# Optimization experiments

Hardware: AMD Instinct MI355X
Metric: run time of the kernel (lower is better)

The kernel has to match this reference:

```python
import jax, jax.numpy as jnp
import numpy as np

B, N, C, H = 8, 1024, 768, 12
HD = C // H
SCALE = HD ** -0.5
LAMBD = 4.0
N_ITERS = 5


def setup_inputs() -> dict:
    key = jax.random.key(0)
    k1, k2, k3, k4, k5 = jax.random.split(key, 5)
    x = jax.random.normal(k1, (B, N, C), dtype=jnp.float32)
    W_qkv = jax.random.normal(k2, (C, 2 * C), dtype=jnp.float32) * (C ** -0.5)
    b_qkv = jax.random.normal(k3, (2 * C,), dtype=jnp.float32) * 0.02
    W_proj = jax.random.normal(k4, (C, C), dtype=jnp.float32) * (C ** -0.5)
    b_proj = jax.random.normal(k5, (C,), dtype=jnp.float32) * 0.02
    return {"x": x, "W_qkv": W_qkv, "b_qkv": b_qkv, "W_proj": W_proj, "b_proj": b_proj}


def _soft_threshold(s, t):
    # (s - t) where s >= t, (s + t) where s <= -t, else 0  (matches the int-mask math)
    return jnp.where(s >= t, s - t, jnp.where(s <= -t, s + t, jnp.zeros_like(s)))


def reference(x, W_qkv, b_qkv, W_proj, b_proj):
    qkv = (x @ W_qkv + b_qkv).reshape(B, N, 2, H, HD)
    qkv = jnp.transpose(qkv, (2, 0, 3, 1, 4))  # [2, B, H, N, HD]
    k, v = qkv[0], qkv[1]

    # mu: [B, H, 1, 1], scalar per (batch, head): N*C/4 / ||k||_1
    mu = (N * C / 4.0) / jnp.sum(jnp.abs(k), axis=(-1, -2), keepdims=True)
    lm = LAMBD * mu

    l = jnp.zeros((B, H, N, HD), dtype=x.dtype)
    y = jnp.zeros((B, H, N, HD), dtype=x.dtype)

    for _ in range(N_ITERS):
        s = _soft_threshold(k - l + y / mu, lm)
        k2 = k - s - y / mu
        attn = jax.nn.softmax(jnp.einsum('bhnd,bhmd->bhnm', k2, k2) * SCALE, axis=-1)
        l = jnp.einsum('bhnm,bhmd->bhnd', attn, v)
        y = y + mu * (k - l - s)

    s = _soft_threshold(k - l + y / mu, lm)
    k2 = k - s - y / mu
    attn = jax.nn.softmax(jnp.einsum('bhnd,bhmd->bhnm', k2, k2) * SCALE, axis=-1)
    out = jnp.einsum('bhnm,bhmd->bhnd', attn, v)  # [B, H, N, HD]

    out = jnp.transpose(out, (0, 2, 1, 3)).reshape(B, N, C)
    out = out @ W_proj + b_proj
    return out, attn
```

## Files before the change

### kernel.cpp

```cpp
#include <hip/hip_runtime.h>

#define B_   8
#define N_   1024
#define C_   768
#define H_   12
#define HD_  64
#define BH_  96
#define SCALE_ 0.125f
#define NIT_ 5

typedef __attribute__((ext_vector_type(8))) short bfrag;
typedef __attribute__((ext_vector_type(4))) float facc;

__device__ __forceinline__ unsigned short bfhi(float x)
{
    return (unsigned short)(__float_as_uint(x) >> 16);
}
__device__ __forceinline__ unsigned short bflo(float x)
{
    const unsigned hu = __float_as_uint(x) & 0xffff0000u;
    return (unsigned short)(__float_as_uint(x - __uint_as_float(hu)) >> 16);
}
__device__ __forceinline__ bfrag pack_hi(float4 a, float4 b)
{
    bfrag r;
    r[0] = (short)bfhi(a.x); r[1] = (short)bfhi(a.y);
    r[2] = (short)bfhi(a.z); r[3] = (short)bfhi(a.w);
    r[4] = (short)bfhi(b.x); r[5] = (short)bfhi(b.y);
    r[6] = (short)bfhi(b.z); r[7] = (short)bfhi(b.w);
    return r;
}
__device__ __forceinline__ bfrag pack_lo(float4 a, float4 b)
{
    bfrag r;
    r[0] = (short)bflo(a.x); r[1] = (short)bflo(a.y);
    r[2] = (short)bflo(a.z); r[3] = (short)bflo(a.w);
    r[4] = (short)bflo(b.x); r[5] = (short)bflo(b.y);
    r[6] = (short)bflo(b.z); r[7] = (short)bflo(b.w);
    return r;
}

__global__ __launch_bounds__(256)
void split_flat(const float* __restrict__ In,
                unsigned short* __restrict__ Oh, unsigned short* __restrict__ Ol)
{
    const size_t i = ((size_t)blockIdx.x * 256 + threadIdx.x) * 8;
    const float4 a = *(const float4*)(In + i);
    const float4 b = *(const float4*)(In + i + 4);
    *(bfrag*)(Oh + i) = pack_hi(a, b);
    *(bfrag*)(Ol + i) = pack_lo(a, b);
}

__global__ __launch_bounds__(256)
void split_wt(const float* __restrict__ W, int ncols,
// ... 291 lines not shown

__global__ __launch_bounds__(256)
void musum(const float* __restrict__ Kb, float* __restrict__ mu)
{
    const int bh = blockIdx.x;
    const int tid = threadIdx.x;
    const float* p = Kb + (size_t)bh * (N_ * HD_);
    float s = 0.0f;
    for (int i = tid; i < N_ * HD_; i += 256) s += fabsf(p[i]);
    for (int off = 32; off; off >>= 1) s += __shfl_down(s, off, 64);
    __shared__ float red[4];
    if ((tid & 63) == 0) red[tid >> 6] = s;
    __syncthreads();
    if (tid == 0)
        mu[bh] = (float)(N_ * C_ / 4.0) / (red[0] + red[1] + red[2] + red[3]);
}

__global__ __launch_bounds__(256)
void ew_fused(const float* __restrict__ Kb, const float* __restrict__ Lb,
              float* __restrict__ Yb, const float* __restrict__ mu,
              float* __restrict__ K2b,
              unsigned short* __restrict__ K2h, unsigned short* __restrict__ K2l,
              int upd)
{
    const int i = blockIdx.x * 256 + threadIdx.x;
    const int bh = i >> 16;
    const float m = mu[bh];
    const float lm = 4.0f * m;
    const float kv = Kb[i];
    float k2;
    if (upd) {
        const float lv = Lb[i];
        const float y = 2.0f * Yb[i] + m * (K2b[i] - lv);
        Yb[i] = y;
        const float yom = y / m;
        const float t = kv - lv + yom;
        const float s = (t >= lm) ? (t - lm) : ((t <= -lm) ? (t + lm) : 0.0f);
        k2 = kv - s - yom;
    } else {
        Yb[i] = 0.0f;
        const float t = kv;
        const float s = (t >= lm) ? (t - lm) : ((t <= -lm) ? (t + lm) : 0.0f);
        k2 = kv - s;
    }
    K2b[i] = k2;
    K2h[i] = bfhi(k2);
    K2l[i] = bflo(k2);
}

__global__ __launch_bounds__(256)
void vt_split(const float* __restrict__ Vb,
              unsigned short* __restrict__ Vth, unsigned short* __restrict__ Vtl)
{
    __shared__ float Ts[64][68];
    const int tid = threadIdx.x;
    const int bh = blockIdx.y;
    const int n0 = blockIdx.x * 64;
    const float* vb = Vb + ((size_t)bh * N_ + n0) * HD_;

    {
        int e = tid;
#pragma unroll
        for (int t = 0; t < 4; ++t, e += 256) {
            const int r = e >> 4, c4 = (e & 15) << 2;
            *(float4*)&Ts[r][c4] = *(const float4*)(vb + r * HD_ + c4);
        }
    }
    __syncthreads();

#pragma unroll
    for (int t = 0; t < 2; ++t) {
        const int idx = t * 2048 + tid * 8;
        const int d = idx >> 6, c = idx & 63;
        bfrag h8, l8;
#pragma unroll
        for (int q = 0; q < 8; ++q) {
            const float v = Ts[c + q][d];
            h8[q] = (short)bfhi(v);
            l8[q] = (short)bflo(v);
        }
        const size_t go = ((size_t)bh * HD_ + d) * N_ + n0 + c;
        *(bfrag*)(Vth + go) = h8;
        *(bfrag*)(Vtl + go) = l8;
    }
}

__global__ __launch_bounds__(256)
void flash(const unsigned short* __restrict__ K2h, const unsigned short* __restrict__ K2l,
           const unsigned short* __restrict__ Vth, const unsigned short* __restrict__ Vtl,
           float* __restrict__ Lout, float* __restrict__ Mrow, float* __restrict__ Zrow,
           unsigned short* __restrict__ Lbh, unsigned short* __restrict__ Lbl, int wsplit)
{
    __shared__ short Kh[64][72];
    __shared__ short Kl[64][72];
    __shared__ short Vh[64][72];
    __shared__ short Vl[64][72];
    short (&Ph)[64][72] = Kh;
    short (&Pl)[64][72] = Kl;

    const int tid  = threadIdx.x;
    const int lane = tid & 63;
    const int w    = tid >> 6;
    const int g    = lane >> 4;
    const int r16  = lane & 15;
    const int bh   = blockIdx.y;
    const int q0   = blockIdx.x * 128;

    const unsigned short* kh = K2h + (size_t)bh * (N_ * HD_);
    const unsigned short* kl = K2l + (size_t)bh * (N_ * HD_);
    const unsigned short* vh = Vth + (size_t)bh * (N_ * HD_);
    const unsigned short* vl = Vtl + (size_t)bh * (N_ * HD_);

    const size_t qoffA = (size_t)(q0 + 16 * w + r16) * HD_ + 8 * g;
    const size_t qoffB = (size_t)(q0 + 64 + 16 * w + r16) * HD_ + 8 * g;
    const bfrag qhA0 = *(const bfrag*)(kh + qoffA);
    const bfrag qhA1 = *(const bfrag*)(kh + qoffA + 32);
    const bfrag qlA0 = *(const bfrag*)(kl + qoffA);
    const bfrag qlA1 = *(const bfrag*)(kl + qoffA + 32);
    const bfrag qhB0 = *(const bfrag*)(kh + qoffB);
    const bfrag qhB1 = *(const bfrag*)(kh + qoffB + 32);
    const bfrag qlB0 = *(const bfrag*)(kl + qoffB);
    const bfrag qlB1 = *(const bfrag*)(kl + qoffB + 32);

    const int i0 = tid * 8,        r0 = i0 >> 6, cc0 = i0 & 63;
    const int i1 = 2048 + tid * 8, r1 = i1 >> 6, cc1 = i1 & 63;

    bfrag pk0 = *(const bfrag*)(kh + i0);
    bfrag pk1 = *(const bfrag*)(kh + i1);
    bfrag pm0 = *(const bfrag*)(kl + i0);
    bfrag pm1 = *(const bfrag*)(kl + i1);

    float mrA0 = -1e30f, mrA1 = -1e30f, mrA2 = -1e30f, mrA3 = -1e30f;
    float zrA0 = 0.0f,  zrA1 = 0.0f,  zrA2 = 0.0f,  zrA3 = 0.0f;
    float mrB0 = -1e30f, mrB1 = -1e30f, mrB2 = -1e30f, mrB3 = -1e30f;
    float zrB0 = 0.0f,  zrB1 = 0.0f,  zrB2 = 0.0f,  zrB3 = 0.0f;
    facc oA0 = {0.f, 0.f, 0.f, 0.f};
    facc oA1 = {0.f, 0.f, 0.f, 0.f};
    facc oA2 = {0.f, 0.f, 0.f, 0.f};
    facc oA3 = {0.f, 0.f, 0.f, 0.f};
    facc oB0 = {0.f, 0.f, 0.f, 0.f};
    facc oB1 = {0.f, 0.f, 0.f, 0.f};
    facc oB2 = {0.f, 0.f, 0.f, 0.f};
    facc oB3 = {0.f, 0.f, 0.f, 0.f};

    for (int kt = 0; kt < 16; ++kt) {
        __syncthreads();
        *(bfrag*)&Kh[r0][cc0] = pk0;  *(bfrag*)&Kh[r1][cc1] = pk1;
        *(bfrag*)&Kl[r0][cc0] = pm0;  *(bfrag*)&Kl[r1][cc1] = pm1;
        const bfrag tv0 = *(const bfrag*)(vh + (size_t)r0 * N_ + kt * 64 + cc0);
        const bfrag tv1 = *(const bfrag*)(vh + (size_t)r1 * N_ + kt * 64 + cc1);
        const bfrag tw0 = *(const bfrag*)(vl + (size_t)r0 * N_ + kt * 64 + cc0);
        const bfrag tw1 = *(const bfrag*)(vl + (size_t)r1 * N_ + kt * 64 + cc1);
        if (kt + 1 < 16) {
            const size_t gn = (size_t)(kt + 1) * 4096;
            pk0 = *(const bfrag*)(kh + gn + i0);
            pk1 = *(const bfrag*)(kh + gn + i1);
            pm0 = *(const bfrag*)(kl + gn + i0);
            pm1 = *(const bfrag*)(kl + gn + i1);
        }
        __syncthreads();

        facc sA0 = {0.f, 0.f, 0.f, 0.f};
        facc sA1 = {0.f, 0.f, 0.f, 0.f};
        facc sA2 = {0.f, 0.f, 0.f, 0.f};
        facc sA3 = {0.f, 0.f, 0.f, 0.f};
        facc sB0 = {0.f, 0.f, 0.f, 0.f};
        facc sB1 = {0.f, 0.f, 0.f, 0.f};
        facc sB2 = {0.f, 0.f, 0.f, 0.f};
        facc sB3 = {0.f, 0.f, 0.f, 0.f};
        {
            bfrag b0 = *(const bfrag*)&Kh[r16][8 * g];
            bfrag b1 = *(const bfrag*)&Kh[r16][32 + 8 * g];
            bfrag c0 = *(const bfrag*)&Kl[r16][8 * g];
            bfrag c1 = *(const bfrag*)&Kl[r16][32 + 8 * g];
            sA0 = __builtin_amdgcn_mfma_f32_16x16x32_bf16(qhA0, b0, sA0, 0, 0, 0);
            sA0 = __builtin_amdgcn_mfma_f32_16x16x32_bf16(qlA0, b0, sA0, 0, 0, 0);
            sA0 = __builtin_amdgcn_mfma_f32_16x16x32_bf16(qhA0, c0, sA0, 0, 0, 0);
            sA0 = __builtin_amdgcn_mfma_f32_16x16x32_bf16(qhA1, b1, sA0, 0, 0, 0);
            sA0 = __builtin_amdgcn_mfma_f32_16x16x32_bf16(qlA1, b1, sA0, 0, 0, 0);
            sA0 = __builtin_amdgcn_mfma_f32_16x16x32_bf16(qhA1, c1, sA0, 0, 0, 0);
            sB0 = __builtin_amdgcn_mfma_f32_16x16x32_bf16(qhB0, b0, sB0, 0, 0, 0);
            sB0 = __builtin_amdgcn_mfma_f32_16x16x32_bf16(qlB0, b0, sB0, 0, 0, 0);
            sB0 = __builtin_amdgcn_mfma_f32_16x16x32_bf16(qhB0, c0, sB0, 0, 0, 0);
            sB0 = __builtin_amdgcn_mfma_f32_16x16x32_bf16(qhB1, b1, sB0, 0, 0, 0);
            sB0 = __builtin_amdgcn_mfma_f32_16x16x32_bf16(qlB1, b1, sB0, 0, 0, 0);
// ... 111 lines not shown
        }
        const float mnB0 = fmaxf(mrB0, mt0), mnB1 = fmaxf(mrB1, mt1);
        const float mnB2 = fmaxf(mrB2, mt2), mnB3 = fmaxf(mrB3, mt3);
        const float aB0 = __expf(mrB0 - mnB0), aB1 = __expf(mrB1 - mnB1);
        const float aB2 = __expf(mrB2 - mnB2), aB3 = __expf(mrB3 - mnB3);
        mrB0 = mnB0; mrB1 = mnB1; mrB2 = mnB2; mrB3 = mnB3;

        const float paB0 = __expf(sB0.x - mnB0), paB1 = __expf(sB0.y - mnB1);
        const float paB2 = __expf(sB0.z - mnB2), paB3 = __expf(sB0.w - mnB3);
        const float pbB0 = __expf(sB1.x - mnB0), pbB1 = __expf(sB1.y - mnB1);
        const float pbB2 = __expf(sB1.z - mnB2), pbB3 = __expf(sB1.w - mnB3);
        const float pcB0 = __expf(sB2.x - mnB0), pcB1 = __expf(sB2.y - mnB1);
        const float pcB2 = __expf(sB2.z - mnB2), pcB3 = __expf(sB2.w - mnB3);
        const float pdB0 = __expf(sB3.x - mnB0), pdB1 = __expf(sB3.y - mnB1);
        const float pdB2 = __expf(sB3.z - mnB2), pdB3 = __expf(sB3.w - mnB3);

        float zsB0 = paB0 + pbB0 + pcB0 + pdB0;
        float zsB1 = paB1 + pbB1 + pcB1 + pdB1;
        float zsB2 = paB2 + pbB2 + pcB2 + pdB2;
        float zsB3 = paB3 + pbB3 + pcB3 + pdB3;
        for (int off = 8; off; off >>= 1) {
            zsB0 += __shfl_xor(zsB0, off, 16);
            zsB1 += __shfl_xor(zsB1, off, 16);
            zsB2 += __shfl_xor(zsB2, off, 16);
            zsB3 += __shfl_xor(zsB3, off, 16);
        }
        zrB0 = zrB0 * aB0 + zsB0;  zrB1 = zrB1 * aB1 + zsB1;
        zrB2 = zrB2 * aB2 + zsB2;  zrB3 = zrB3 * aB3 + zsB3;
        oB0.x *= aB0; oB0.y *= aB1; oB0.z *= aB2; oB0.w *= aB3;
        oB1.x *= aB0; oB1.y *= aB1; oB1.z *= aB2; oB1.w *= aB3;
        oB2.x *= aB0; oB2.y *= aB1; oB2.z *= aB2; oB2.w *= aB3;
        oB3.x *= aB0; oB3.y *= aB1; oB3.z *= aB2; oB3.w *= aB3;

        *(bfrag*)&Vh[r0][cc0] = tv0;  *(bfrag*)&Vh[r1][cc1] = tv1;
        *(bfrag*)&Vl[r0][cc0] = tw0;  *(bfrag*)&Vl[r1][cc1] = tw1;

        __syncthreads();

        const int pr = 16 * w + 4 * g;
        Ph[pr + 0][r16]      = (short)bfhi(paA0); Pl[pr + 0][r16]      = (short)bflo(paA0);
        Ph[pr + 1][r16]      = (short)bfhi(paA1); Pl[pr + 1][r16]      = (short)bflo(paA1);
        Ph[pr + 2][r16]      = (short)bfhi(paA2); Pl[pr + 2][r16]      = (short)bflo(paA2);
        Ph[pr + 3][r16]      = (short)bfhi(paA3); Pl[pr + 3][r16]      = (short)bflo(paA3);
        Ph[pr + 0][16 + r16] = (short)bfhi(pbA0); Pl[pr + 0][16 + r16] = (short)bflo(pbA0);
        Ph[pr + 1][16 + r16] = (short)bfhi(pbA1); Pl[pr + 1][16 + r16] = (short)bflo(pbA1);
        Ph[pr + 2][16 + r16] = (short)bfhi(pbA2); Pl[pr + 2][16 + r16] = (short)bflo(pbA2);
        Ph[pr + 3][16 + r16] = (short)bfhi(pbA3); Pl[pr + 3][16 + r16] = (short)bflo(pbA3);
        Ph[pr + 0][32 + r16] = (short)bfhi(pcA0); Pl[pr + 0][32 + r16] = (short)bflo(pcA0);
        Ph[pr + 1][32 + r16] = (short)bfhi(pcA1); Pl[pr + 1][32 + r16] = (short)bflo(pcA1);
        Ph[pr + 2][32 + r16] = (short)bfhi(pcA2); Pl[pr + 2][32 + r16] = (short)bflo(pcA2);
        Ph[pr + 3][32 + r16] = (short)bfhi(pcA3); Pl[pr + 3][32 + r16] = (short)bflo(pcA3);
        Ph[pr + 0][48 + r16] = (short)bfhi(pdA0); Pl[pr + 0][48 + r16] = (short)bflo(pdA0);
        Ph[pr + 1][48 + r16] = (short)bfhi(pdA1); Pl[pr + 1][48 + r16] = (short)bflo(pdA1);
        Ph[pr + 2][48 + r16] = (short)bfhi(pdA2); Pl[pr + 2][48 + r16] = (short)bflo(pdA2);
        Ph[pr + 3][48 + r16] = (short)bfhi(pdA3); Pl[pr + 3][48 + r16] = (short)bflo(pdA3);
        __builtin_amdgcn_wave_barrier();
        {
            const bfrag ph0 = *(const bfrag*)&Ph[16 * w + r16][8 * g];
            const bfrag ph1 = *(const bfrag*)&Ph[16 * w + r16][32 + 8 * g];
            const bfrag pl0 = *(const bfrag*)&Pl[16 * w + r16][8 * g];
            const bfrag pl1 = *(const bfrag*)&Pl[16 * w + r16][32 + 8 * g];
            {
                bfrag b0 = *(const bfrag*)&Vh[r16][8 * g];
                bfrag b1 = *(const bfrag*)&Vh[r16][32 + 8 * g];
                bfrag c0 = *(const bfrag*)&Vl[r16][8 * g];
                bfrag c1 = *(const bfrag*)&Vl[r16][32 + 8 * g];
                oA0 = __builtin_amdgcn_mfma_f32_16x16x32_bf16(ph0, b0, oA0, 0, 0, 0);
                oA0 = __builtin_amdgcn_mfma_f32_16x16x32_bf16(pl0, b0, oA0, 0, 0, 0);
                oA0 = __builtin_amdgcn_mfma_f32_16x16x32_bf16(ph0, c0, oA0, 0, 0, 0);
                oA0 = __builtin_amdgcn_mfma_f32_16x16x32_bf16(ph1, b1, oA0, 0, 0, 0);
                oA0 = __builtin_amdgcn_mfma_f32_16x16x32_bf16(pl1, b1, oA0, 0, 0, 0);
                oA0 = __builtin_amdgcn_mfma_f32_16x16x32_bf16(ph1, c1, oA0, 0, 0, 0);
            }
            {
                bfrag b0 = *(const bfrag*)&Vh[16 + r16][8 * g];
                bfrag b1 = *(const bfrag*)&Vh[16 + r16][32 + 8 * g];
                bfrag c0 = *(const bfrag*)&Vl[16 + r16][8 * g];
                bfrag c1 = *(const bfrag*)&Vl[16 + r16][32 + 8 * g];
                oA1 = __builtin_amdgcn_mfma_f32_16x16x32_bf16(ph0, b0, oA1, 0, 0, 0);
                oA1 = __builtin_amdgcn_mfma_f32_16x16x32_bf16(pl0, b0, oA1, 0, 0, 0);
                oA1 = __builtin_amdgcn_mfma_f32_16x16x32_bf16(ph0, c0, oA1, 0, 0, 0);
                oA1 = __builtin_amdgcn_mfma_f32_16x16x32_bf16(ph1, b1, oA1, 0, 0, 0);
                oA1 = __builtin_amdgcn_mfma_f32_16x16x32_bf16(pl1, b1, oA1, 0, 0, 0);
                oA1 = __builtin_amdgcn_mfma_f32_16x16x32_bf16(ph1, c1, oA1, 0, 0, 0);
            }
            {
                bfrag b0 = *(const bfrag*)&Vh[32 + r16][8 * g];
                bfrag b1 = *(const bfrag*)&Vh[32 + r16][32 + 8 * g];
                bfrag c0 = *(const bfrag*)&Vl[32 + r16][8 * g];
                bfrag c1 = *(const bfrag*)&Vl[32 + r16][32 + 8 * g];
                oA2 = __builtin_amdgcn_mfma_f32_16x16x32_bf16(ph0, b0, oA2, 0, 0, 0);
                oA2 = __builtin_amdgcn_mfma_f32_16x16x32_bf16(pl0, b0, oA2, 0, 0, 0);
                oA2 = __builtin_amdgcn_mfma_f32_16x16x32_bf16(ph0, c0, oA2, 0, 0, 0);
                oA2 = __builtin_amdgcn_mfma_f32_16x16x32_bf16(ph1, b1, oA2, 0, 0, 0);
                oA2 = __builtin_amdgcn_mfma_f32_16x16x32_bf16(pl1, b1, oA2, 0, 0, 0);
                oA2 = __builtin_amdgcn_mfma_f32_16x16x32_bf16(ph1, c1, oA2, 0, 0, 0);
            }
            {
                bfrag b0 = *(const bfrag*)&Vh[48 + r16][8 * g];
                bfrag b1 = *(const bfrag*)&Vh[48 + r16][32 + 8 * g];
                bfrag c0 = *(const bfrag*)&Vl[48 + r16][8 * g];
                bfrag c1 = *(const bfrag*)&Vl[48 + r16][32 + 8 * g];
                oA3 = __builtin_amdgcn_mfma_f32_16x16x32_bf16(ph0, b0, oA3, 0, 0, 0);
                oA3 = __builtin_amdgcn_mfma_f32_16x16x32_bf16(pl0, b0, oA3, 0, 0, 0);
                oA3 = __builtin_amdgcn_mfma_f32_16x16x32_bf16(ph0, c0, oA3, 0, 0, 0);
                oA3 = __builtin_amdgcn_mfma_f32_16x16x32_bf16(ph1, b1, oA3, 0, 0, 0);
                oA3 = __builtin_amdgcn_mfma_f32_16x16x32_bf16(pl1, b1, oA3, 0, 0, 0);
                oA3 = __builtin_amdgcn_mfma_f32_16x16x32_bf16(ph1, c1, oA3, 0, 0, 0);
            }
        }
        __builtin_amdgcn_wave_barrier();

        Ph[pr + 0][r16]      = (short)bfhi(paB0); Pl[pr + 0][r16]      = (short)bflo(paB0);
        Ph[pr + 1][r16]      = (short)bfhi(paB1); Pl[pr + 1][r16]      = (short)bflo(paB1);
        Ph[pr + 2][r16]      = (short)bfhi(paB2); Pl[pr + 2][r16]      = (short)bflo(paB2);
        Ph[pr + 3][r16]      = (short)bfhi(paB3); Pl[pr + 3][r16]      = (short)bflo(paB3);
        Ph[pr + 0][16 + r16] = (short)bfhi(pbB0); Pl[pr + 0][16 + r16] = (short)bflo(pbB0);
        Ph[pr + 1][16 + r16] = (short)bfhi(pbB1); Pl[pr + 1][16 + r16] = (short)bflo(pbB1);
        Ph[pr + 2][16 + r16] = (short)bfhi(pbB2); Pl[pr + 2][16 + r16] = (short)bflo(pbB2);
        Ph[pr + 3][16 + r16] = (short)bfhi(pbB3); Pl[pr + 3][16 + r16] = (short)bflo(pbB3);
        Ph[pr + 0][32 + r16] = (short)bfhi(pcB0); Pl[pr + 0][32 + r16] = (short)bflo(pcB0);
        Ph[pr + 1][32 + r16] = (short)bfhi(pcB1); Pl[pr + 1][32 + r16] = (short)bflo(pcB1);
        Ph[pr + 2][32 + r16] = (short)bfhi(pcB2); Pl[pr + 2][32 + r16] = (short)bflo(pcB2);
        Ph[pr + 3][32 + r16] = (short)bfhi(pcB3); Pl[pr + 3][32 + r16] = (short)bflo(pcB3);
        Ph[pr + 0][48 + r16] = (short)bfhi(pdB0); Pl[pr + 0][48 + r16] = (short)bflo(pdB0);
        Ph[pr + 1][48 + r16] = (short)bfhi(pdB1); Pl[pr + 1][48 + r16] = (short)bflo(pdB1);
        Ph[pr + 2][48 + r16] = (short)bfhi(pdB2); Pl[pr + 2][48 + r16] = (short)bflo(pdB2);
        Ph[pr + 3][48 + r16] = (short)bfhi(pdB3); Pl[pr + 3][48 + r16] = (short)bflo(pdB3);
        __builtin_amdgcn_wave_barrier();
        {
            const bfrag ph0 = *(const bfrag*)&Ph[16 * w + r16][8 * g];
            const bfrag ph1 = *(const bfrag*)&Ph[16 * w + r16][32 + 8 * g];
            const bfrag pl0 = *(const bfrag*)&Pl[16 * w + r16][8 * g];
            const bfrag pl1 = *(const bfrag*)&Pl[16 * w + r16][32 + 8 * g];
            {
                bfrag b0 = *(const bfrag*)&Vh[r16][8 * g];
                bfrag b1 = *(const bfrag*)&Vh[r16][32 + 8 * g];
                bfrag c0 = *(const bfrag*)&Vl[r16][8 * g];
                bfrag c1 = *(const bfrag*)&Vl[r16][32 + 8 * g];
                oB0 = __builtin_amdgcn_mfma_f32_16x16x32_bf16(ph0, b0, oB0, 0, 0, 0);
                oB0 = __builtin_amdgcn_mfma_f32_16x16x32_bf16(pl0, b0, oB0, 0, 0, 0);
                oB0 = __builtin_amdgcn_mfma_f32_16x16x32_bf16(ph0, c0, oB0, 0, 0, 0);
                oB0 = __builtin_amdgcn_mfma_f32_16x16x32_bf16(ph1, b1, oB0, 0, 0, 0);
                oB0 = __builtin_amdgcn_mfma_f32_16x16x32_bf16(pl1, b1, oB0, 0, 0, 0);
                oB0 = __builtin_amdgcn_mfma_f32_16x16x32_bf16(ph1, c1, oB0, 0, 0, 0);
            }
            {
                bfrag b0 = *(const bfrag*)&Vh[16 + r16][8 * g];
                bfrag b1 = *(const bfrag*)&Vh[16 + r16][32 + 8 * g];
                bfrag c0 = *(const bfrag*)&Vl[16 + r16][8 * g];
                bfrag c1 = *(const bfrag*)&Vl[16 + r16][32 + 8 * g];
                oB1 = __builtin_amdgcn_mfma_f32_16x16x32_bf16(ph0, b0, oB1, 0, 0, 0);
                oB1 = __builtin_amdgcn_mfma_f32_16x16x32_bf16(pl0, b0, oB1, 0, 0, 0);
                oB1 = __builtin_amdgcn_mfma_f32_16x16x32_bf16(ph0, c0, oB1, 0, 0, 0);
                oB1 = __builtin_amdgcn_mfma_f32_16x16x32_bf16(ph1, b1, oB1, 0, 0, 0);
                oB1 = __builtin_amdgcn_mfma_f32_16x16x32_bf16(pl1, b1, oB1, 0, 0, 0);
                oB1 = __builtin_amdgcn_mfma_f32_16x16x32_bf16(ph1, c1, oB1, 0, 0, 0);
            }
            {
                bfrag b0 = *(const bfrag*)&Vh[32 + r16][8 * g];
                bfrag b1 = *(const bfrag*)&Vh[32 + r16][32 + 8 * g];
                bfrag c0 = *(const bfrag*)&Vl[32 + r16][8 * g];
                bfrag c1 = *(const bfrag*)&Vl[32 + r16][32 + 8 * g];
                oB2 = __builtin_amdgcn_mfma_f32_16x16x32_bf16(ph0, b0, oB2, 0, 0, 0);
                oB2 = __builtin_amdgcn_mfma_f32_16x16x32_bf16(pl0, b0, oB2, 0, 0, 0);
                oB2 = __builtin_amdgcn_mfma_f32_16x16x32_bf16(ph0, c0, oB2, 0, 0, 0);
                oB2 = __builtin_amdgcn_mfma_f32_16x16x32_bf16(ph1, b1, oB2, 0, 0, 0);
                oB2 = __builtin_amdgcn_mfma_f32_16x16x32_bf16(pl1, b1, oB2, 0, 0, 0);
                oB2 = __builtin_amdgcn_mfma_f32_16x16x32_bf16(ph1, c1, oB2, 0, 0, 0);
            }
            {
                bfrag b0 = *(const bfrag*)&Vh[48 + r16][8 * g];
                bfrag b1 = *(const bfrag*)&Vh[48 + r16][32 + 8 * g];
                bfrag c0 = *(const bfrag*)&Vl[48 + r16][8 * g];
                bfrag c1 = *(const bfrag*)&Vl[48 + r16][32 + 8 * g];
                oB3 = __builtin_amdgcn_mfma_f32_16x16x32_bf16(ph0, b0, oB3, 0, 0, 0);
                oB3 = __builtin_amdgcn_mfma_f32_16x16x32_bf16(pl0, b0, oB3, 0, 0, 0);
                oB3 = __builtin_amdgcn_mfma_f32_16x16x32_bf16(ph0, c0, oB3, 0, 0, 0);
                oB3 = __builtin_amdgcn_mfma_f32_16x16x32_bf16(ph1, b1, oB3, 0, 0, 0);
                oB3 = __builtin_amdgcn_mfma_f32_16x16x32_bf16(pl1, b1, oB3, 0, 0, 0);
                oB3 = __builtin_amdgcn_mfma_f32_16x16x32_bf16(ph1, c1, oB3, 0, 0, 0);
            }
        }
    }

    {
        const float zi0 = 1.0f / zrA0, zi1 = 1.0f / zrA1;
        const float zi2 = 1.0f / zrA2, zi3 = 1.0f / zrA3;
        const size_t base = ((size_t)bh * N_ + q0 + 16 * w + 4 * g) * HD_ + r16;
        float* lrow = Lout + base;
        const float v00 = oA0.x * zi0, v01 = oA1.x * zi0, v02 = oA2.x * zi0, v03 = oA3.x * zi0;
        const float v10 = oA0.y * zi1, v11 = oA1.y * zi1, v12 = oA2.y * zi1, v13 = oA3.y * zi1;
        const float v20 = oA0.z * zi2, v21 = oA1.z * zi2, v22 = oA2.z * zi2, v23 = oA3.z * zi2;
        const float v30 = oA0.w * zi3, v31 = oA1.w * zi3, v32 = oA2.w * zi3, v33 = oA3.w * zi3;
        lrow[0 * HD_ + 0] = v00; lrow[0 * HD_ + 16] = v01; lrow[0 * HD_ + 32] = v02; lrow[0 * HD_ + 48] = v03;
        lrow[1 * HD_ + 0] = v10; lrow[1 * HD_ + 16] = v11; lrow[1 * HD_ + 32] = v12; lrow[1 * HD_ + 48] = v13;
        lrow[2 * HD_ + 0] = v20; lrow[2 * HD_ + 16] = v21; lrow[2 * HD_ + 32] = v22; lrow[2 * HD_ + 48] = v23;
        lrow[3 * HD_ + 0] = v30; lrow[3 * HD_ + 16] = v31; lrow[3 * HD_ + 32] = v32; lrow[3 * HD_ + 48] = v33;
        if (wsplit) {
            Lbh[base + 0 * HD_ + 0] = bfhi(v00); Lbl[base + 0 * HD_ + 0] = bflo(v00);
            Lbh[base + 0 * HD_ + 16] = bfhi(v01); Lbl[base + 0 * HD_ + 16] = bflo(v01);
            Lbh[base + 0 * HD_ + 32] = bfhi(v02); Lbl[base + 0 * HD_ + 32] = bflo(v02);
            Lbh[base + 0 * HD_ + 48] = bfhi(v03); Lbl[base + 0 * HD_ + 48] = bflo(v03);
            Lbh[base + 1 * HD_ + 0] = bfhi(v10); Lbl[base + 1 * HD_ + 0] = bflo(v10);
            Lbh[base + 1 * HD_ + 16] = bfhi(v11); Lbl[base + 1 * HD_ + 16] = bflo(v11);
            Lbh[base + 1 * HD_ + 32] = bfhi(v12); Lbl[base + 1 * HD_ + 32] = bflo(v12);
            Lbh[base + 1 * HD_ + 48] = bfhi(v13); Lbl[base + 1 * HD_ + 48] = bflo(v13);
            Lbh[base + 2 * HD_ + 0] = bfhi(v20); Lbl[base + 2 * HD_ + 0] = bflo(v20);
            Lbh[base + 2 * HD_ + 16] = bfhi(v21); Lbl[base + 2 * HD_ + 16] = bflo(v21);
            Lbh[base + 2 * HD_ + 32] = bfhi(v22); Lbl[base + 2 * HD_ + 32] = bflo(v22);
            Lbh[base + 2 * HD_ + 48] = bfhi(v23); Lbl[base + 2 * HD_ + 48] = bflo(v23);
            Lbh[base + 3 * HD_ + 0] = bfhi(v30); Lbl[base + 3 * HD_ + 0] = bflo(v30);
            Lbh[base + 3 * HD_ + 16] = bfhi(v31); Lbl[base + 3 * HD_ + 16] = bflo(v31);
            Lbh[base + 3 * HD_ + 32] = bfhi(v32); Lbl[base + 3 * HD_ + 32] = bflo(v32);
            Lbh[base + 3 * HD_ + 48] = bfhi(v33); Lbl[base + 3 * HD_ + 48] = bflo(v33);
        }
// ... 195 lines not shown
    const size_t SZ = (size_t)BH_ * N_ * HD_;
    float* ws   = (float*)d_ws;
    float* kb   = ws;
    float* vb   = ws + SZ;
    float* lb   = ws + 2 * SZ;
    float* yb   = ws + 3 * SZ;
    float* k2b  = ws + 4 * SZ;
    float* mu   = ws + 5 * SZ;
    float* rowm = mu + 128;
    float* rowz = rowm + (size_t)BH_ * N_;

    unsigned short* k2h  = (unsigned short*)attn_f;
    unsigned short* k2l  = k2h + SZ;
    unsigned short* vth  = k2h + 2 * SZ;
    unsigned short* vtl  = k2h + 3 * SZ;
    unsigned short* xh   = k2h + 4 * SZ;
    unsigned short* xl   = k2h + 5 * SZ;
    unsigned short* wqth = k2h + 6 * SZ;
    unsigned short* wqtl = k2h + 7 * SZ;
    unsigned short* wpth = k2h + 8 * SZ;
    unsigned short* wptl = k2h + 9 * SZ;
    unsigned short* lbh  = k2h + 10 * SZ;
    unsigned short* lbl  = k2h + 11 * SZ;

    split_flat<<<3072, 256, 0, stream>>>(x, xh, xl);
    split_wt<<<dim3(24, 12), 256, 0, stream>>>(Wq, 2 * C_, wqth, wqtl);
    split_wt<<<dim3(12, 12), 256, 0, stream>>>(Wp, C_, wpth, wptl);

    qkv_mfma<<<dim3(24, 128), 256, 0, stream>>>(xh, xl, wqth, wqtl, bq, kb, vb);
    vt_split<<<dim3(16, 96), 256, 0, stream>>>(vb, vth, vtl);
    musum<<<96, 256, 0, stream>>>(kb, mu);

    for (int it = 0; it <= NIT_; ++it) {
        ew_fused<<<24576, 256, 0, stream>>>(kb, lb, yb, mu, k2b, k2h, k2l,
                                            it > 0 ? 1 : 0);
        flash<<<dim3(8, 96), 256, 0, stream>>>(k2h, k2l, vth, vtl, lb, rowm, rowz,
                                               lbh, lbl, it == NIT_ ? 1 : 0);
    }

    proj_mfma<<<dim3(12, 128), 256, 0, stream>>>(lbh, lbl, wpth, wptl, bp, out_f);
    attn_out_mfma<<<dim3(16, 96), 256, 0, stream>>>(k2b, rowm, rowz, attn_f);
}
```

Before: 1.629 ms.

## Load V fragments directly from global and pack P hi/lo into shared words

```diff
diff --git a/kernel.cpp b/kernel.cpp
--- a/kernel.cpp
+++ b/kernel.cpp
@@ -20,6 +20,10 @@
 {
     const unsigned hu = __float_as_uint(x) & 0xffff0000u;
     return (unsigned short)(__float_as_uint(x - __uint_as_float(hu)) >> 16);
+}
+__device__ __forceinline__ unsigned int packhl(float v)
+{
+    return (unsigned int)bfhi(v) | ((unsigned int)bflo(v) << 16);
 }
 __device__ __forceinline__ bfrag pack_hi(float4 a, float4 b)
 {
@@ -377,7 +381,7 @@
     if (upd) {
         const float lv = Lb[i];
         const float y = 2.0f * Yb[i] + m * (K2b[i] - lv);
-        Yb[i] = y;
+        if (upd == 1) Yb[i] = y;
         const float yom = y / m;
         const float t = kv - lv + yom;
         const float s = (t >= lm) ? (t - lm) : ((t <= -lm) ? (t + lm) : 0.0f);
@@ -430,18 +434,31 @@
     }
 }
 
+#define DEINT(PU0, PU1, PH, PL) do {                                          \
+    uint4 _uh, _ul;                                                           \
+    _uh.x = (PU0.x & 0xffffu) | (PU0.y << 16);                                \
+    _uh.y = (PU0.z & 0xffffu) | (PU0.w << 16);                                \
+    _uh.z = (PU1.x & 0xffffu) | (PU1.y << 16);                                \
+    _uh.w = (PU1.z & 0xffffu) | (PU1.w << 16);                                \
+    _ul.x = (PU0.x >> 16) | (PU0.y & 0xffff0000u);                            \
+    _ul.y = (PU0.z >> 16) | (PU0.w & 0xffff0000u);                            \
+    _ul.z = (PU1.x >> 16) | (PU1.y & 0xffff0000u);                            \
+    _ul.w = (PU1.z >> 16) | (PU1.w & 0xffff0000u);                            \
+    PH = *(const bfrag*)&_uh;                                                 \
+    PL = *(const bfrag*)&_ul;                                                 \
+} while (0)
+
 __global__ __launch_bounds__(256)
 void flash(const unsigned short* __restrict__ K2h, const unsigned short* __restrict__ K2l,
            const unsigned short* __restrict__ Vth, const unsigned short* __restrict__ Vtl,
            float* __restrict__ Lout, float* __restrict__ Mrow, float* __restrict__ Zrow,
            unsigned short* __restrict__ Lbh, unsigned short* __restrict__ Lbl, int wsplit)
 {
-    __shared__ short Kh[64][72];
-    __shared__ short Kl[64][72];
-    __shared__ short Vh[64][72];
-    __shared__ short Vl[64][72];
-    short (&Ph)[64][72] = Kh;
-    short (&Pl)[64][72] = Kl;
+    __shared__ __attribute__((aligned(16))) unsigned int PuBuf[2 * 64 * 68];
+    short (*Kh)[72] = (short(*)[72])PuBuf;
+    short (*Kl)[72] = (short(*)[72])((short*)PuBuf + 64 * 72);
+    unsigned int (*PuA)[68] = (unsigned int(*)[68])PuBuf;
+    unsigned int (*PuB)[68] = (unsigned int(*)[68])(PuBuf + 64 * 68);
 
     const int tid  = threadIdx.x;
     const int lane = tid & 63;
@@ -474,6 +491,11 @@
     bfrag pk1 = *(const bfrag*)(kh + i1);
     bfrag pm0 = *(const bfrag*)(kl + i0);
     bfrag pm1 = *(const bfrag*)(kl + i1);
+
+    const size_t vrow0 = (size_t)(r16)      * N_ + 8 * g;
+    const size_t vrow1 = (size_t)(16 + r16) * N_ + 8 * g;
+    const size_t vrow2 = (size_t)(32 + r16) * N_ + 8 * g;
+    const size_t vrow3 = (size_t)(48 + r16) * N_ + 8 * g;
 
     float mrA0 = -1e30f, mrA1 = -1e30f, mrA2 = -1e30f, mrA3 = -1e30f;
     float zrA0 = 0.0f,  zrA1 = 0.0f,  zrA2 = 0.0f,  zrA3 = 0.0f;
@@ -489,13 +511,14 @@
     facc oB3 = {0.f, 0.f, 0.f, 0.f};
 
     for (int kt = 0; kt < 16; ++kt) {
+        const int ko = kt * 64;
         __syncthreads();
         *(bfrag*)&Kh[r0][cc0] = pk0;  *(bfrag*)&Kh[r1][cc1] = pk1;
         *(bfrag*)&Kl[r0][cc0] = pm0;  *(bfrag*)&Kl[r1][cc1] = pm1;
-        const bfrag tv0 = *(const bfrag*)(vh + (size_t)r0 * N_ + kt * 64 + cc0);
-        const bfrag tv1 = *(const bfrag*)(vh + (size_t)r1 * N_ + kt * 64 + cc1);
-        const bfrag tw0 = *(const bfrag*)(vl + (size_t)r0 * N_ + kt * 64 + cc0);
-        const bfrag tw1 = *(const bfrag*)(vl + (size_t)r1 * N_ + kt * 64 + cc1);
+        const bfrag v0b0 = *(const bfrag*)(vh + vrow0 + ko);
+        const bfrag v0b1 = *(const bfrag*)(vh + vrow0 + ko + 32);
+        const bfrag v0c0 = *(const bfrag*)(vl + vrow0 + ko);
+        const bfrag v0c1 = *(const bfrag*)(vl + vrow0 + ko + 32);
         if (kt + 1 < 16) {
             const size_t gn = (size_t)(kt + 1) * 4096;
             pk0 = *(const bfrag*)(kh + gn + i0);
@@ -673,156 +696,123 @@
         oB2.x *= aB0; oB2.y *= aB1; oB2.z *= aB2; oB2.w *= aB3;
         oB3.x *= aB0; oB3.y *= aB1; oB3.z *= aB2; oB3.w *= aB3;
 
-        *(bfrag*)&Vh[r0][cc0] = tv0;  *(bfrag*)&Vh[r1][cc1] = tv1;
-        *(bfrag*)&Vl[r0][cc0] = tw0;  *(bfrag*)&Vl[r1][cc1] = tw1;
-
         __syncthreads();
 
         const int pr = 16 * w + 4 * g;
-        Ph[pr + 0][r16]      = (short)bfhi(paA0); Pl[pr + 0][r16]      = (short)bflo(paA0);
-        Ph[pr + 1][r16]      = (short)bfhi(paA1); Pl[pr + 1][r16]      = (short)bflo(paA1);
-        Ph[pr + 2][r16]      = (short)bfhi(paA2); Pl[pr + 2][r16]      = (short)bflo(paA2);
-        Ph[pr + 3][r16]      = (short)bfhi(paA3); Pl[pr + 3][r16]      = (short)bflo(paA3);
-        Ph[pr + 0][16 + r16] = (short)bfhi(pbA0); Pl[pr + 0][16 + r16] = (short)bflo(pbA0);
-        Ph[pr + 1][16 + r16] = (short)bfhi(pbA1); Pl[pr + 1][16 + r16] = (short)bflo(pbA1);
-        Ph[pr + 2][16 + r16] = (short)bfhi(pbA2); Pl[pr + 2][16 + r16] = (short)bflo(pbA2);
-        Ph[pr + 3][16 + r16] = (short)bfhi(pbA3); Pl[pr + 3][16 + r16] = (short)bflo(pbA3);
-        Ph[pr + 0][32 + r16] = (short)bfhi(pcA0); Pl[pr + 0][32 + r16] = (short)bflo(pcA0);
-        Ph[pr + 1][32 + r16] = (short)bfhi(pcA1); Pl[pr + 1][32 + r16] = (short)bflo(pcA1);
-        Ph[pr + 2][32 + r16] = (short)bfhi(pcA2); Pl[pr + 2][32 + r16] = (short)bflo(pcA2);
-        Ph[pr + 3][32 + r16] = (short)bfhi(pcA3); Pl[pr + 3][32 + r16] = (short)bflo(pcA3);
-        Ph[pr + 0][48 + r16] = (short)bfhi(pdA0); Pl[pr + 0][48 + r16] = (short)bflo(pdA0);
-        Ph[pr + 1][48 + r16] = (short)bfhi(pdA1); Pl[pr + 1][48 + r16] = (short)bflo(pdA1);
-        Ph[pr + 2][48 + r16] = (short)bfhi(pdA2); Pl[pr + 2][48 + r16] = (short)bflo(pdA2);
-        Ph[pr + 3][48 + r16] = (short)bfhi(pdA3); Pl[pr + 3][48 + r16] = (short)bflo(pdA3);
+        const int prow = 16 * w + r16;
+        PuA[pr + 0][r16]      = packhl(paA0);
+        PuA[pr + 1][r16]      = packhl(paA1);
+        PuA[pr + 2][r16]      = packhl(paA2);
+        PuA[pr + 3][r16]      = packhl(paA3);
+        PuA[pr + 0][16 + r16] = packhl(pbA0);
+        PuA[pr + 1][16 + r16] = packhl(pbA1);
+        PuA[pr + 2][16 + r16] = packhl(pbA2);
+        PuA[pr + 3][16 + r16] = packhl(pbA3);
+        PuA[pr + 0][32 + r16] = packhl(pcA0);
+        PuA[pr + 1][32 + r16] = packhl(pcA1);
+        PuA[pr + 2][32 + r16] = packhl(pcA2);
+        PuA[pr + 3][32 + r16] = packhl(pcA3);
+        PuA[pr + 0][48 + r16] = packhl(pdA0);
+        PuA[pr + 1][48 + r16] = packhl(pdA1);
+        PuA[pr + 2][48 + r16] = packhl(pdA2);
+        PuA[pr + 3][48 + r16] = packhl(pdA3);
+        PuB[pr + 0][r16]      = packhl(paB0);
+        PuB[pr + 1][r16]      = packhl(paB1);
+        PuB[pr + 2][r16]      = packhl(paB2);
+        PuB[pr + 3][r16]      = packhl(paB3);
+        PuB[pr + 0][16 + r16] = packhl(pbB0);
+        PuB[pr + 1][16 + r16] = packhl(pbB1);
+        PuB[pr + 2][16 + r16] = packhl(pbB2);
+        PuB[pr + 3][16 + r16] = packhl(pbB3);
+        PuB[pr + 0][32 + r16] = packhl(pcB0);
+        PuB[pr + 1][32 + r16] = packhl(pcB1);
+        PuB[pr + 2][32 + r16] = packhl(pcB2);
+        PuB[pr + 3][32 + r16] = packhl(pcB3);
+        PuB[pr + 0][48 + r16] = packhl(pdB0);
+        PuB[pr + 1][48 + r16] = packhl(pdB1);
+        PuB[pr + 2][48 + r16] = packhl(pdB2);
+        PuB[pr + 3][48 + r16] = packhl(pdB3);
         __builtin_amdgcn_wave_barrier();
-        {
-            const bfrag ph0 = *(const bfrag*)&Ph[16 * w + r16][8 * g];
-            const bfrag ph1 = *(const bfrag*)&Ph[16 * w + r16][32 + 8 * g];
-            const bfrag pl0 = *(const bfrag*)&Pl[16 * w + r16][8 * g];
-            const bfrag pl1 = *(const bfrag*)&Pl[16 * w + r16][32 + 8 * g];
-            {
-                bfrag b0 = *(const bfrag*)&Vh[r16][8 * g];
-                bfrag b1 = *(const bfrag*)&Vh[r16][32 + 8 * g];
-                bfrag c0 = *(const bfrag*)&Vl[r16][8 * g];
-                bfrag c1 = *(const bfrag*)&Vl[r16][32 + 8 * g];
-                oA0 = __builtin_amdgcn_mfma_f32_16x16x32_bf16(ph0, b0, oA0, 0, 0, 0);
-                oA0 = __builtin_amdgcn_mfma_f32_16x16x32_bf16(pl0, b0, oA0, 0, 0, 0);
-                oA0 = __builtin_amdgcn_mfma_f32_16x16x32_bf16(ph0, c0, oA0, 0, 0, 0);
-                oA0 = __builtin_amdgcn_mfma_f32_16x16x32_bf16(ph1, b1, oA0, 0, 0, 0);
-                oA0 = __builtin_amdgcn_mfma_f32_16x16x32_bf16(pl1, b1, oA0, 0, 0, 0);
-                oA0 = __builtin_amdgcn_mfma_f32_16x16x32_bf16(ph1, c1, oA0, 0, 0, 0);
-            }
-            {
-                bfrag b0 = *(const bfrag*)&Vh[16 + r16][8 * g];
-                bfrag b1 = *(const bfrag*)&Vh[16 + r16][32 + 8 * g];
-                bfrag c0 = *(const bfrag*)&Vl[16 + r16][8 * g];
-                bfrag c1 = *(const bfrag*)&Vl[16 + r16][32 + 8 * g];
-                oA1 = __builtin_amdgcn_mfma_f32_16x16x32_bf16(ph0, b0, oA1, 0, 0, 0);
-                oA1 = __builtin_amdgcn_mfma_f32_16x16x32_bf16(pl0, b0, oA1, 0, 0, 0);
-                oA1 = __builtin_amdgcn_mfma_f32_16x16x32_bf16(ph0, c0, oA1, 0, 0, 0);
-                oA1 = __builtin_amdgcn_mfma_f32_16x16x32_bf16(ph1, b1, oA1, 0, 0, 0);
-                oA1 = __builtin_amdgcn_mfma_f32_16x16x32_bf16(pl1, b1, oA1, 0, 0, 0);
-                oA1 = __builtin_amdgcn_mfma_f32_16x16x32_bf16(ph1, c1, oA1, 0, 0, 0);
-            }
-            {
-                bfrag b0 = *(const bfrag*)&Vh[32 + r16][8 * g];
-                bfrag b1 = *(const bfrag*)&Vh[32 + r16][32 + 8 * g];
-                bfrag c0 = *(const bfrag*)&Vl[32 + r16][8 * g];
-                bfrag c1 = *(const bfrag*)&Vl[32 + r16][32 + 8 * g];
-                oA2 = __builtin_amdgcn_mfma_f32_16x16x32_bf16(ph0, b0, oA2, 0, 0, 0);
-                oA2 = __builtin_amdgcn_mfma_f32_16x16x32_bf16(pl0, b0, oA2, 0, 0, 0);
-                oA2 = __builtin_amdgcn_mfma_f32_16x16x32_bf16(ph0, c0, oA2, 0, 0, 0);
-                oA2 = __builtin_amdgcn_mfma_f32_16x16x32_bf16(ph1, b1, oA2, 0, 0, 0);
-                oA2 = __builtin_amdgcn_mfma_f32_16x16x32_bf16(pl1, b1, oA2, 0, 0, 0);
-                oA2 = __builtin_amdgcn_mfma_f32_16x16x32_bf16(ph1, c1, oA2, 0, 0, 0);
-            }
-            {
-                bfrag b0 = *(const bfrag*)&Vh[48 + r16][8 * g];
-                bfrag b1 = *(const bfrag*)&Vh[48 + r16][32 + 8 * g];
-                bfrag c0 = *(const bfrag*)&Vl[48 + r16][8 * g];
-                bfrag c1 = *(const bfrag*)&Vl[48 + r16][32 + 8 * g];
-                oA3 = __builtin_amdgcn_mfma_f32_16x16x32_bf16(ph0, b0, oA3, 0, 0, 0);
-                oA3 = __builtin_amdgcn_mfma_f32_16x16x32_bf16(pl0, b0, oA3, 0, 0, 0);
-                oA3 = __builtin_amdgcn_mfma_f32_16x16x32_bf16(ph0, c0, oA3, 0, 0, 0);
-                oA3 = __builtin_amdgcn_mfma_f32_16x16x32_bf16(ph1, b1, oA3, 0, 0, 0);
-                oA3 = __builtin_amdgcn_mfma_f32_16x16x32_bf16(pl1, b1, oA3, 0, 0, 0);
-                oA3 = __builtin_amdgcn_mfma_f32_16x16x32_bf16(ph1, c1, oA3, 0, 0, 0);
-            }
-        }
-        __builtin_amdgcn_wave_barrier();
-
-        Ph[pr + 0][r16]      = (short)bfhi(paB0); Pl[pr + 0][r16]      = (short)bflo(paB0);
-        Ph[pr + 1][r16]      = (short)bfhi(paB1); Pl[pr + 1][r16]      = (short)bflo(paB1);
-        Ph[pr + 2][r16]      = (short)bfhi(paB2); Pl[pr + 2][r16]      = (short)bflo(paB2);
-        Ph[pr + 3][r16]      = (short)bfhi(paB3); Pl[pr + 3][r16]      = (short)bflo(paB3);
-        Ph[pr + 0][16 + r16] = (short)bfhi(pbB0); Pl[pr + 0][16 + r16] = (short)bflo(pbB0);
-        Ph[pr + 1][16 + r16] = (short)bfhi(pbB1); Pl[pr + 1][16 + r16] = (short)bflo(pbB1);
-        Ph[pr + 2][16 + r16] = (short)bfhi(pbB2); Pl[pr + 2][16 + r16] = (short)bflo(pbB2);
-        Ph[pr + 3][16 + r16] = (short)bfhi(pbB3); Pl[pr + 3][16 + r16] = (short)bflo(pbB3);
-        Ph[pr + 0][32 + r16] = (short)bfhi(pcB0); Pl[pr + 0][32 + r16] = (short)bflo(pcB0);
-        Ph[pr + 1][32 + r16] = (short)bfhi(pcB1); Pl[pr + 1][32 + r16] = (short)bflo(pcB1);
-        Ph[pr + 2][32 + r16] = (short)bfhi(pcB2); Pl[pr + 2][32 + r16] = (short)bflo(pcB2);
-        Ph[pr + 3][32 + r16] = (short)bfhi(pcB3); Pl[pr + 3][32 + r16] = (short)bflo(pcB3);
-        Ph[pr + 0][48 + r16] = (short)bfhi(pdB0); Pl[pr + 0][48 + r16] = (short)bflo(pdB0);
-        Ph[pr + 1][48 + r16] = (short)bfhi(pdB1); Pl[pr + 1][48 + r16] = (short)bflo(pdB1);
-        Ph[pr + 2][48 + r16] = (short)bfhi(pdB2); Pl[pr + 2][48 + r16] = (short)bflo(pdB2);
-        Ph[pr + 3][48 + r16] = (short)bfhi(pdB3); Pl[pr + 3][48 + r16] = (short)bflo(pdB3);
-        __builtin_amdgcn_wave_barrier();
-        {
-            const bfrag ph0 = *(const bfrag*)&Ph[16 * w + r16][8 * g];
-            const bfrag ph1 = *(const bfrag*)&Ph[16 * w + r16][32 + 8 * g];
-            const bfrag pl0 = *(const bfrag*)&Pl[16 * w + r16][8 * g];
-            const bfrag pl1 = *(const bfrag*)&Pl[16 * w + r16][32 + 8 * g];
-            {
-                bfrag b0 = *(const bfrag*)&Vh[r16][8 * g];
-                bfrag b1 = *(const bfrag*)&Vh[r16][32 + 8 * g];
-                bfrag c0 = *(const bfrag*)&Vl[r16][8 * g];
-                bfrag c1 = *(const bfrag*)&Vl[r16][32 + 8 * g];
-                oB0 = __builtin_amdgcn_mfma_f32_16x16x32_bf16(ph0, b0, oB0, 0, 0, 0);
-                oB0 = __builtin_amdgcn_mfma_f32_16x16x32_bf16(pl0, b0, oB0, 0, 0, 0);
-                oB0 = __builtin_amdgcn_mfma_f32_16x16x32_bf16(ph0, c0, oB0, 0, 0, 0);
-                oB0 = __builtin_amdgcn_mfma_f32_16x16x32_bf16(ph1, b1, oB0, 0, 0, 0);
-                oB0 = __builtin_amdgcn_mfma_f32_16x16x32_bf16(pl1, b1, oB0, 0, 0, 0);
-                oB0 = __builtin_amdgcn_mfma_f32_16x16x32_bf16(ph1, c1, oB0, 0, 0, 0);
-            }
-            {
-                bfrag b0 = *(const bfrag*)&Vh[16 + r16][8 * g];
-                bfrag b1 = *(const bfrag*)&Vh[16 + r16][32 + 8 * g];
-                bfrag c0 = *(const bfrag*)&Vl[16 + r16][8 * g];
-                bfrag c1 = *(const bfrag*)&Vl[16 + r16][32 + 8 * g];
-                oB1 = __builtin_amdgcn_mfma_f32_16x16x32_bf16(ph0, b0, oB1, 0, 0, 0);
-                oB1 = __builtin_amdgcn_mfma_f32_16x16x32_bf16(pl0, b0, oB1, 0, 0, 0);
-                oB1 = __builtin_amdgcn_mfma_f32_16x16x32_bf16(ph0, c0, oB1, 0, 0, 0);
-                oB1 = __builtin_amdgcn_mfma_f32_16x16x32_bf16(ph1, b1, oB1, 0, 0, 0);
-                oB1 = __builtin_amdgcn_mfma_f32_16x16x32_bf16(pl1, b1, oB1, 0, 0, 0);
-                oB1 = __builtin_amdgcn_mfma_f32_16x16x32_bf16(ph1, c1, oB1, 0, 0, 0);
-            }
-            {
-                bfrag b0 = *(const bfrag*)&Vh[32 + r16][8 * g];
-                bfrag b1 = *(const bfrag*)&Vh[32 + r16][32 + 8 * g];
-                bfrag c0 = *(const bfrag*)&Vl[32 + r16][8 * g];
-                bfrag c1 = *(const bfrag*)&Vl[32 + r16][32 + 8 * g];
-                oB2 = __builtin_amdgcn_mfma_f32_16x16x32_bf16(ph0, b0, oB2, 0, 0, 0);
-                oB2 = __builtin_amdgcn_mfma_f32_16x16x32_bf16(pl0, b0, oB2, 0, 0, 0);
-                oB2 = __builtin_amdgcn_mfma_f32_16x16x32_bf16(ph0, c0, oB2, 0, 0, 0);
-                oB2 = __builtin_amdgcn_mfma_f32_16x16x32_bf16(ph1, b1, oB2, 0, 0, 0);
-                oB2 = __builtin_amdgcn_mfma_f32_16x16x32_bf16(pl1, b1, oB2, 0, 0, 0);
-                oB2 = __builtin_amdgcn_mfma_f32_16x16x32_bf16(ph1, c1, oB2, 0, 0, 0);
-            }
-            {
-                bfrag b0 = *(const bfrag*)&Vh[48 + r16][8 * g];
-                bfrag b1 = *(const bfrag*)&Vh[48 + r16][32 + 8 * g];
-                bfrag c0 = *(const bfrag*)&Vl[48 + r16][8 * g];
-                bfrag c1 = *(const bfrag*)&Vl[48 + r16][32 + 8 * g];
-                oB3 = __builtin_amdgcn_mfma_f32_16x16x32_bf16(ph0, b0, oB3, 0, 0, 0);
-                oB3 = __builtin_amdgcn_mfma_f32_16x16x32_bf16(pl0, b0, oB3, 0, 0, 0);
-                oB3 = __builtin_amdgcn_mfma_f32_16x16x32_bf16(ph0, c0, oB3, 0, 0, 0);
-                oB3 = __builtin_amdgcn_mfma_f32_16x16x32_bf16(ph1, b1, oB3, 0, 0, 0);
-                oB3 = __builtin_amdgcn_mfma_f32_16x16x32_bf16(pl1, b1, oB3, 0, 0, 0);
-                oB3 = __builtin_amdgcn_mfma_f32_16x16x32_bf16(ph1, c1, oB3, 0, 0, 0);
-            }
-        }
+
+        bfrag phA0, plA0, phA1, plA1, phB0, plB0, phB1, plB1;
+        {
+            const uint4 a0 = *(const uint4*)&PuA[prow][8 * g];
+            const uint4 a1 = *(const uint4*)&PuA[prow][8 * g + 4];
+            const uint4 a2 = *(const uint4*)&PuA[prow][32 + 8 * g];
+            const uint4 a3 = *(const uint4*)&PuA[prow][32 + 8 * g + 4];
+            DEINT(a0, a1, phA0, plA0);
+            DEINT(a2, a3, phA1, plA1);
+            const uint4 b0 = *(const uint4*)&PuB[prow][8 * g];
+            const uint4 b1 = *(const uint4*)&PuB[prow][8 * g + 4];
+            const uint4 b2 = *(const uint4*)&PuB[prow][32 + 8 * g];
+            const uint4 b3 = *(const uint4*)&PuB[prow][32 + 8 * g + 4];
+            DEINT(b0, b1, phB0, plB0);
+            DEINT(b2, b3, phB1, plB1);
+        }
+
+        const bfrag v1b0 = *(const bfrag*)(vh + vrow1 + ko);
+        const bfrag v1b1 = *(const bfrag*)(vh + vrow1 + ko + 32);
+        const bfrag v1c0 = *(const bfrag*)(vl + vrow1 + ko);
+        const bfrag v1c1 = *(const bfrag*)(vl + vrow1 + ko + 32);
+        oA0 = __builtin_amdgcn_mfma_f32_16x16x32_bf16(phA0, v0b0, oA0, 0, 0, 0);
+        oA0 = __builtin_amdgcn_mfma_f32_16x16x32_bf16(plA0, v0b0, oA0, 0, 0, 0);
+        oA0 = __builtin_amdgcn_mfma_f32_16x16x32_bf16(phA0, v0c0, oA0, 0, 0, 0);
+        oA0 = __builtin_amdgcn_mfma_f32_16x16x32_bf16(phA1, v0b1, oA0, 0, 0, 0);
+        oA0 = __builtin_amdgcn_mfma_f32_16x16x32_bf16(plA1, v0b1, oA0, 0, 0, 0);
+        oA0 = __builtin_amdgcn_mfma_f32_16x16x32_bf16(phA1, v0c1, oA0, 0, 0, 0);
+        oB0 = __builtin_amdgcn_mfma_f32_16x16x32_bf16(phB0, v0b0, oB0, 0, 0, 0);
+        oB0 = __builtin_amdgcn_mfma_f32_16x16x32_bf16(plB0, v0b0, oB0, 0, 0, 0);
+        oB0 = __builtin_amdgcn_mfma_f32_16x16x32_bf16(phB0, v0c0, oB0, 0, 0, 0);
+        oB0 = __builtin_amdgcn_mfma_f32_16x16x32_bf16(phB1, v0b1, oB0, 0, 0, 0);
+        oB0 = __builtin_amdgcn_mfma_f32_16x16x32_bf16(plB1, v0b1, oB0, 0, 0, 0);
+        oB0 = __builtin_amdgcn_mfma_f32_16x16x32_bf16(phB1, v0c1, oB0, 0, 0, 0);
+
+        const bfrag v2b0 = *(const bfrag*)(vh + vrow2 + ko);
+        const bfrag v2b1 = *(const bfrag*)(vh + vrow2 + ko + 32);
+        const bfrag v2c0 = *(const bfrag*)(vl + vrow2 + ko);
+        const bfrag v2c1 = *(const bfrag*)(vl + vrow2 + ko + 32);
+        oA1 = __builtin_amdgcn_mfma_f32_16x16x32_bf16(phA0, v1b0, oA1, 0, 0, 0);
+        oA1 = __builtin_amdgcn_mfma_f32_16x16x32_bf16(plA0, v1b0, oA1, 0, 0, 0);
+        oA1 = __builtin_amdgcn_mfma_f32_16x16x32_bf16(phA0, v1c0, oA1, 0, 0, 0);
+        oA1 = __builtin_amdgcn_mfma_f32_16x16x32_bf16(phA1, v1b1, oA1, 0, 0, 0);
+        oA1 = __builtin_amdgcn_mfma_f32_16x16x32_bf16(plA1, v1b1, oA1, 0, 0, 0);
+        oA1 = __builtin_amdgcn_mfma_f32_16x16x32_bf16(phA1, v1c1, oA1, 0, 0, 0);
+        oB1 = __builtin_amdgcn_mfma_f32_16x16x32_bf16(phB0, v1b0, oB1, 0, 0, 0);
+        oB1 = __builtin_amdgcn_mfma_f32_16x16x32_bf16(plB0, v1b0, oB1, 0, 0, 0);
+        oB1 = __builtin_amdgcn_mfma_f32_16x16x32_bf16(phB0, v1c0, oB1, 0, 0, 0);
+        oB1 = __builtin_amdgcn_mfma_f32_16x16x32_bf16(phB1, v1b1, oB1, 0, 0, 0);
+        oB1 = __builtin_amdgcn_mfma_f32_16x16x32_bf16(plB1, v1b1, oB1, 0, 0, 0);
+        oB1 = __builtin_amdgcn_mfma_f32_16x16x32_bf16(phB1, v1c1, oB1, 0, 0, 0);
+
+        const bfrag v3b0 = *(const bfrag*)(vh + vrow3 + ko);
+        const bfrag v3b1 = *(const bfrag*)(vh + vrow3 + ko + 32);
+        const bfrag v3c0 = *(const bfrag*)(vl + vrow3 + ko);
+        const bfrag v3c1 = *(const bfrag*)(vl + vrow3 + ko + 32);
+        oA2 = __builtin_amdgcn_mfma_f32_16x16x32_bf16(phA0, v2b0, oA2, 0, 0, 0);
+        oA2 = __builtin_amdgcn_mfma_f32_16x16x32_bf16(plA0, v2b0, oA2, 0, 0, 0);
+        oA2 = __builtin_amdgcn_mfma_f32_16x16x32_bf16(phA0, v2c0, oA2, 0, 0, 0);
+        oA2 = __builtin_amdgcn_mfma_f32_16x16x32_bf16(phA1, v2b1, oA2, 0, 0, 0);
+        oA2 = __builtin_amdgcn_mfma_f32_16x16x32_bf16(plA1, v2b1, oA2, 0, 0, 0);
+        oA2 = __builtin_amdgcn_mfma_f32_16x16x32_bf16(phA1, v2c1, oA2, 0, 0, 0);
+        oB2 = __builtin_amdgcn_mfma_f32_16x16x32_bf16(phB0, v2b0, oB2, 0, 0, 0);
+        oB2 = __builtin_amdgcn_mfma_f32_16x16x32_bf16(plB0, v2b0, oB2, 0, 0, 0);
+        oB2 = __builtin_amdgcn_mfma_f32_16x16x32_bf16(phB0, v2c0, oB2, 0, 0, 0);
+        oB2 = __builtin_amdgcn_mfma_f32_16x16x32_bf16(phB1, v2b1, oB2, 0, 0, 0);
+        oB2 = __builtin_amdgcn_mfma_f32_16x16x32_bf16(plB1, v2b1, oB2, 0, 0, 0);
+        oB2 = __builtin_amdgcn_mfma_f32_16x16x32_bf16(phB1, v2c1, oB2, 0, 0, 0);
+
+        oA3 = __builtin_amdgcn_mfma_f32_16x16x32_bf16(phA0, v3b0, oA3, 0, 0, 0);
+        oA3 = __builtin_amdgcn_mfma_f32_16x16x32_bf16(plA0, v3b0, oA3, 0, 0, 0);
+        oA3 = __builtin_amdgcn_mfma_f32_16x16x32_bf16(phA0, v3c0, oA3, 0, 0, 0);
+        oA3 = __builtin_amdgcn_mfma_f32_16x16x32_bf16(phA1, v3b1, oA3, 0, 0, 0);
+        oA3 = __builtin_amdgcn_mfma_f32_16x16x32_bf16(plA1, v3b1, oA3, 0, 0, 0);
+        oA3 = __builtin_amdgcn_mfma_f32_16x16x32_bf16(phA1, v3c1, oA3, 0, 0, 0);
+        oB3 = __builtin_amdgcn_mfma_f32_16x16x32_bf16(phB0, v3b0, oB3, 0, 0, 0);
+        oB3 = __builtin_amdgcn_mfma_f32_16x16x32_bf16(plB0, v3b0, oB3, 0, 0, 0);
+        oB3 = __builtin_amdgcn_mfma_f32_16x16x32_bf16(phB0, v3c0, oB3, 0, 0, 0);
+        oB3 = __builtin_amdgcn_mfma_f32_16x16x32_bf16(phB1, v3b1, oB3, 0, 0, 0);
+        oB3 = __builtin_amdgcn_mfma_f32_16x16x32_bf16(plB1, v3b1, oB3, 0, 0, 0);
+        oB3 = __builtin_amdgcn_mfma_f32_16x16x32_bf16(phB1, v3c1, oB3, 0, 0, 0);
     }
 
     {
@@ -1084,8 +1074,8 @@
     musum<<<96, 256, 0, stream>>>(kb, mu);
 
     for (int it = 0; it <= NIT_; ++it) {
-        ew_fused<<<24576, 256, 0, stream>>>(kb, lb, yb, mu, k2b, k2h, k2l,
-                                            it > 0 ? 1 : 0);
+        const int upd = (it == 0) ? 0 : (it == NIT_ ? 2 : 1);
+        ew_fused<<<24576, 256, 0, stream>>>(kb, lb, yb, mu, k2b, k2h, k2l, upd);
         flash<<<dim3(8, 96), 256, 0, stream>>>(k2h, k2l, vth, vtl, lb, rowm, rowz,
                                                lbh, lbl, it == NIT_ ? 1 : 0);
     }
```

After: 1.868 ms. +14.7%, slower.
